# Kernel tuning notes

Hardware: AMD Instinct MI355X
Metric: run time of the kernel (lower is better)

## Reference

```python
import jax, jax.numpy as jnp
import numpy as np

N_NODES = 100000


def _sage_conv(x, edge_index, W_l, W_r, b):
    # PyG SAGEConv (aggr='mean', root_weight=True, bias in lin_l):
    # out_i = W_l @ mean_{j in N(i)} x_j + b + W_r @ x_i
    src = edge_index[0]
    dst = edge_index[1]
    msg = x[src]                                              # [E, d] gather
    agg = jax.ops.segment_sum(msg, dst, num_segments=N_NODES)  # [N, d]
    deg = jax.ops.segment_sum(jnp.ones((src.shape[0],), x.dtype), dst,
                              num_segments=N_NODES)            # [N]
    agg = agg / jnp.maximum(deg, 1.0)[:, None]                 # mean, 0 if isolated
    return agg @ W_l.T + b + x @ W_r.T


def setup_inputs() -> dict:
    key = jax.random.key(0)
    ks = jax.random.split(key, 10)
    E, P = 1600000, 200000
    d_in, d_hid, d_out = 64, 128, 64
    s = 0.05
    return {
        "x": jax.random.normal(ks[0], (N_NODES, d_in), jnp.float32),
        "edge_index": jax.random.randint(ks[1], (2, E), 0, N_NODES, jnp.int32).astype(jnp.int64),
        "pairs": jax.random.randint(ks[2], (P, 2), 0, N_NODES, jnp.int32).astype(jnp.int64),
        "W1l": jax.random.normal(ks[3], (d_hid, d_in), jnp.float32) * s,
        "W1r": jax.random.normal(ks[4], (d_hid, d_in), jnp.float32) * s,
        "b1": jnp.zeros((d_hid,), jnp.float32),
        "W2l": jax.random.normal(ks[5], (d_out, d_hid), jnp.float32) * s,
        "W2r": jax.random.normal(ks[6], (d_out, d_hid), jnp.float32) * s,
        "b2": jnp.zeros((d_out,), jnp.float32),
        "Wlp": jax.random.normal(ks[7], (1, 2 * d_out), jnp.float32) * s,
        "blp": jnp.zeros((1,), jnp.float32),
    }


def reference(x, edge_index, pairs, W1l, W1r, b1, W2l, W2r, b2, Wlp, blp):
    h = _sage_conv(x, edge_index, W1l, W1r, b1)
    h = jax.nn.relu(h)
    h = _sage_conv(h, edge_index, W2l, W2r, b2)          # [N, d_out]
    src_emb = h[pairs[:, 0]]                              # [P, d_out]
    dst_emb = h[pairs[:, 1]]                              # [P, d_out]
    edge_emb = jnp.concatenate([src_emb, dst_emb], axis=1)  # [P, 2*d_out]
    logits = edge_emb @ Wlp.T + blp                       # [P, 1]
    return jax.nn.sigmoid(logits).squeeze(-1)             # [P]
```

## Files before the change

### kernel.cpp

```cpp
#include <hip/hip_runtime.h>


typedef __attribute__((ext_vector_type(8))) short bf16x8;
typedef __attribute__((ext_vector_type(4))) float f32x4;

#define NBLK_A 256

__device__ __forceinline__ unsigned short f2bf(float f) {
    unsigned u = __float_as_uint(f);
    u = u + 0x7fffu + ((u >> 16) & 1u);
    return (unsigned short)(u >> 16);
}
__device__ __forceinline__ float b2f(unsigned short s) {
    return __uint_as_float(((unsigned)s) << 16);
}
__device__ __forceinline__ float uflo(unsigned v) { return __uint_as_float(v << 16); }
__device__ __forceinline__ float ufhi(unsigned v) { return __uint_as_float(v & 0xffff0000u); }

__device__ __forceinline__ long load_idx(const void* p, long i, int is64) {
    if (is64) return (long)((const long long*)p)[i];
    return (long)((const int*)p)[i];
}

__device__ __forceinline__ int detect64_local(const void* p) {
    const unsigned* u = (const unsigned*)p;
    unsigned a = 0;
#pragma unroll
    for (int i = 0; i < 32; ++i) a |= u[2 * i + 1];
    return a == 0u;
}

__global__ void pre_kernel(const void* eidx, const float* __restrict__ x,
                           const float* __restrict__ W1l, const float* __restrict__ W1r,
                           const float* __restrict__ W2l, const float* __restrict__ W2r,
                           const float* __restrict__ b2, const float* __restrict__ Wlp,
                           const float* __restrict__ blp,
                           int* __restrict__ blk_hist, unsigned short* __restrict__ xaown,
                           unsigned short* __restrict__ w1bf, float* __restrict__ wv,
                           int* __restrict__ flag,
                           long N, long E, int NBK, int chunk, int xcb) {
    int b = blockIdx.x;
    int tid = threadIdx.x;
    if (b < NBLK_A) {
        __shared__ int h[512];
        for (int i = tid; i < NBK; i += 256) h[i] = 0;
        __syncthreads();
        int is64 = detect64_local(eidx);
        long e0 = (long)b * chunk;
        long e1 = e0 + chunk; if (e1 > E) e1 = E;
        for (long e = e0 + tid; e < e1; e += 256) {
            long dst = load_idx(eidx, E + e, is64);
            atomicAdd(&h[(int)(dst >> 8)], 1);
        }
        __syncthreads();
        for (int i = tid; i < NBK; i += 256) blk_hist[i * NBLK_A + b] = h[i];
    } else if (b < NBLK_A + xcb) {
        long t = (long)(b - NBLK_A) * 256 + tid;
        long n = t >> 4;
        int q = (int)(t & 15);
        if (n >= N) return;
        float4 v = *(const float4*)&x[n * 64 + q * 4];
        uint2 u;
        u.x = (unsigned)f2bf(v.x) | ((unsigned)f2bf(v.y) << 16);
        u.y = (unsigned)f2bf(v.z) | ((unsigned)f2bf(v.w) << 16);
        *(uint2*)&xaown[n * 64 + q * 4] = u;
    } else {
        if (tid == 0) *flag = detect64_local(eidx);
        if (tid < 128) {
            int k = tid;
            float s0 = 0.f, s1 = 0.f, s2 = 0.f, s3 = 0.f;
            for (int o = 0; o < 64; ++o) {
                float wl = Wlp[o], wr = Wlp[64 + o];
                float l = W2l[o * 128 + k], r = W2r[o * 128 + k];
                s0 += wl * l; s1 += wr * l; s2 += wl * r; s3 += wr * r;
            }
            wv[k] = s0; wv[128 + k] = s1; wv[256 + k] = s2; wv[384 + k] = s3;
            if (k == 0) {
                float c = blp[0];
                for (int o = 0; o < 64; ++o) c += (Wlp[o] + Wlp[64 + o]) * b2[o];
                wv[512] = c;
            }
        }
        for (int i = tid; i < 16384; i += 256) {
            int o = i >> 7, k = i & 127;
            float f = (k < 64) ? W1l[o * 64 + k] : W1r[o * 64 + (k - 64)];
            w1bf[i ^ ((o & 7) << 3)] = f2bf(f);
        }
    }
}

__global__ void bucket_relscan_kernel(int* __restrict__ blk_hist, int* __restrict__ total) {
    __shared__ int ts[256];
    int k = blockIdx.x, t = threadIdx.x;
    int v = blk_hist[k * NBLK_A + t];
    ts[t] = v; __syncthreads();
    for (int off = 1; off < 256; off <<= 1) {
        int u = (t >= off) ? ts[t - off] : 0;
        __syncthreads();
        ts[t] += u;
        __syncthreads();
    }
    blk_hist[k * NBLK_A + t] = ts[t] - v;
    if (t == 255) total[k] = ts[255];
}

__global__ void base_kernel(const int* __restrict__ total, int* __restrict__ base,
                            int* __restrict__ row_start, int NBK, long N, long E) {
    __shared__ int ts[256];
    int t = threadIdx.x;
    int a = (t < NBK) ? total[t] : 0;
    int b = (256 + t < NBK) ? total[256 + t] : 0;
    ts[t] = a; __syncthreads();
    for (int off = 1; off < 256; off <<= 1) {
        int u = (t >= off) ? ts[t - off] : 0;
        __syncthreads();
        ts[t] += u;
        __syncthreads();
    }
    int incl1 = ts[t];
    int sum1 = ts[255];
    if (t < NBK) base[t] = incl1 - a;
    __syncthreads();
    ts[t] = b; __syncthreads();
    for (int off = 1; off < 256; off <<= 1) {
        int u = (t >= off) ? ts[t - off] : 0;
        __syncthreads();
        ts[t] += u;
        __syncthreads();
    }
    int incl2 = ts[t];
    if (256 + t < NBK) base[256 + t] = sum1 + incl2 - b;
    if (t == 255) base[NBK] = sum1 + incl2;
    if (t == 0) row_start[N] = (int)E;
}

__global__ void bucket_scatter_kernel(const void* eidx, const int* flag,
                                      const int* __restrict__ blk_hist, const int* __restrict__ base,
                                      unsigned* __restrict__ ebuf, long E, int NBK, int chunk) {
    __shared__ int cur[512];
    int tid = threadIdx.x, b = blockIdx.x;
    for (int i = tid; i < NBK; i += 256) cur[i] = blk_hist[i * NBLK_A + b] + base[i];
    __syncthreads();
    int is64 = *flag;
    long e0 = (long)b * chunk;
    long e1 = e0 + chunk; if (e1 > E) e1 = E;
    for (long e = e0 + tid; e < e1; e += 256) {
        long src = load_idx(eidx, e, is64);
        long dst = load_idx(eidx, E + e, is64);
        int pos = atomicAdd(&cur[(int)(dst >> 8)], 1);
        ebuf[pos] = (unsigned)src | ((unsigned)(dst & 255) << 24);
    }
}

__global__ void bucket_csr_kernel(const unsigned* __restrict__ ebuf, const int* __restrict__ base,
                                  int* __restrict__ csr_src, int* __restrict__ row_start, long N) {
    __shared__ int cnt[256], sc[256], cur[256];
    int k = blockIdx.x, t = threadIdx.x;
    int bstart = base[k], bend = base[k + 1];
    cnt[t] = 0;
    __syncthreads();
    for (int i = bstart + t; i < bend; i += 256)
        atomicAdd(&cnt[ebuf[i] >> 24], 1);
    __syncthreads();
    int c = cnt[t];
    sc[t] = c; __syncthreads();
    for (int off = 1; off < 256; off <<= 1) {
        int u = (t >= off) ? sc[t - off] : 0;
        __syncthreads();
        sc[t] += u;
        __syncthreads();
    }
    int loff = sc[t] - c;
    cur[t] = loff;
    long n = (long)k * 256 + t;
    if (n < N) row_start[n] = bstart + loff;
    __syncthreads();
    for (int i = bstart + t; i < bend; i += 256) {
        unsigned v = ebuf[i];
        int dl = (int)(v >> 24);
        int p = atomicAdd(&cur[dl], 1);
        csr_src[bstart + p] = (int)(v & 0xFFFFFFu);
    }
}

__global__ __launch_bounds__(512, 4) void fused_gg_kernel(
        const int* __restrict__ rs, const int* __restrict__ csr,
        const unsigned short* __restrict__ xaown,
        const unsigned short* __restrict__ w1bf, const float* __restrict__ b1,
        const float* __restrict__ wv,
        float* __restrict__ ab, float* __restrict__ cd, long N) {
    __shared__ __align__(16) unsigned short wbuf[128 * 128];
    __shared__ __align__(16) unsigned short aggt[8][16 * 64];
    __shared__ float bs1[128];
    __shared__ float wvs[512];
    int tid = threadIdx.x;

    {
        const uint4* src = (const uint4*)w1bf;
        uint4* dst = (uint4*)wbuf;
#pragma unroll
        for (int i = 0; i < 4; ++i) dst[tid + i * 512] = src[tid + i * 512];
    }
    if (tid < 128) bs1[tid] = b1[tid];
    wvs[tid] = wv[tid];

    int lane = tid & 63, wid = tid >> 6;
    int l16 = lane & 15, lg = lane >> 4;
    long n0 = (long)blockIdx.x * 128 + wid * 16;
    unsigned short* agg = aggt[wid];
    unsigned boff = (unsigned)l16 * 4u;

    for (int nl = 0; nl < 16; ++nl) {
        long n = n0 + nl;
        int s = 0, e = 0;
        if (n < N) { s = rs[n]; e = rs[n + 1]; }
        float a0 = 0.f, a1 = 0.f, a2 = 0.f, a3 = 0.f;
        int j = s;
        for (; j + 16 <= e; j += 16) {
            unsigned o0 = ((unsigned)csr[j + lg] << 6) | boff;
            unsigned o1 = ((unsigned)csr[j + 4 + lg] << 6) | boff;
            unsigned o2 = ((unsigned)csr[j + 8 + lg] << 6) | boff;
            unsigned o3 = ((unsigned)csr[j + 12 + lg] << 6) | boff;
            uint2 r0 = *(const uint2*)&xaown[o0];
            uint2 r1 = *(const uint2*)&xaown[o1];
            uint2 r2 = *(const uint2*)&xaown[o2];
            uint2 r3 = *(const uint2*)&xaown[o3];
            a0 += uflo(r0.x); a1 += ufhi(r0.x); a2 += uflo(r0.y); a3 += ufhi(r0.y);
            a0 += uflo(r1.x); a1 += ufhi(r1.x); a2 += uflo(r1.y); a3 += ufhi(r1.y);
            a0 += uflo(r2.x); a1 += ufhi(r2.x); a2 += uflo(r2.y); a3 += ufhi(r2.y);
            a0 += uflo(r3.x); a1 += ufhi(r3.x); a2 += uflo(r3.y); a3 += ufhi(r3.y);
        }
        if (j < e) {
#pragma unroll
            for (int t = 0; t < 4; ++t) {
                int pos = j + 4 * t + lg;
                int ok = pos < e;
                unsigned oo = ((unsigned)csr[ok ? pos : s] << 6) | boff;
                uint2 r = *(const uint2*)&xaown[oo];
                float m = ok ? 1.f : 0.f;
                a0 += m * uflo(r.x); a1 += m * ufhi(r.x);
                a2 += m * uflo(r.y); a3 += m * ufhi(r.y);
            }
        }
        a0 += __shfl_xor(a0, 16, 64);  a1 += __shfl_xor(a1, 16, 64);
        a2 += __shfl_xor(a2, 16, 64);  a3 += __shfl_xor(a3, 16, 64);
        a0 += __shfl_xor(a0, 32, 64);  a1 += __shfl_xor(a1, 32, 64);
        a2 += __shfl_xor(a2, 32, 64);  a3 += __shfl_xor(a3, 32, 64);
        if (lg == 0) {
            float inv = 1.0f / fmaxf((float)(e - s), 1.0f);
            uint2 o;
            o.x = (unsigned)f2bf(a0 * inv) | ((unsigned)f2bf(a1 * inv) << 16);
            o.y = (unsigned)f2bf(a2 * inv) | ((unsigned)f2bf(a3 * inv) << 16);
            int eo = (l16 * 4) ^ ((nl & 7) << 3);
            *(uint2*)&agg[nl * 64 + eo] = o;
        }
    }
    __syncthreads();

    f32x4 acc[8];
#pragma unroll
    for (int ot = 0; ot < 8; ++ot) acc[ot] = (f32x4){0.f, 0.f, 0.f, 0.f};
    const unsigned short* A0 = xaown + (n0 + l16) * 64;
#pragma unroll
    for (int ks = 0; ks < 4; ++ks) {
        int k0 = ks * 32;
        bf16x8 a;
        if (ks < 2) a = *(const bf16x8*)&agg[l16 * 64 + ((k0 + 8 * lg) ^ ((l16 & 7) << 3))];
        else        a = *(const bf16x8*)&A0[(k0 - 64) + 8 * lg];
#pragma unroll
        for (int ot = 0; ot < 8; ++ot) {
            int o = ot * 16 + l16;
            bf16x8 b = *(const bf16x8*)&wbuf[(o * 128 + k0 + 8 * lg) ^ ((o & 7) << 3)];
            acc[ot] = __builtin_amdgcn_mfma_f32_16x16x32_bf16(a, b, acc[ot], 0, 0, 0);
        }
    }

#pragma unroll
    for (int j = 0; j < 4; ++j) {
        float da = 0.f, db = 0.f, dc = 0.f, dd = 0.f;
#pragma unroll
        for (int ot = 0; ot < 8; ++ot) {
            int col = ot * 16 + l16;
            float hv = fmaxf(acc[ot][j] + bs1[col], 0.f);
            da += hv * wvs[col];       db += hv * wvs[128 + col];
            dc += hv * wvs[256 + col]; dd += hv * wvs[384 + col];
        }
        da += __shfl_xor(da, 1, 64); db += __shfl_xor(db, 1, 64);
        dc += __shfl_xor(dc, 1, 64); dd += __shfl_xor(dd, 1, 64);
        da += __shfl_xor(da, 2, 64); db += __shfl_xor(db, 2, 64);
        dc += __shfl_xor(dc, 2, 64); dd += __shfl_xor(dd, 2, 64);
        da += __shfl_xor(da, 4, 64); db += __shfl_xor(db, 4, 64);
        dc += __shfl_xor(dc, 4, 64); dd += __shfl_xor(dd, 4, 64);
        da += __shfl_xor(da, 8, 64); db += __shfl_xor(db, 8, 64);
        dc += __shfl_xor(dc, 8, 64); dd += __shfl_xor(dd, 8, 64);
        long n = n0 + lg * 4 + j;
        if (l16 == 0 && n < N) {
            *(float2*)&ab[n * 2] = make_float2(da, db);
            *(float2*)&cd[n * 2] = make_float2(dc, dd);
        }
    }
}

__global__ void sgather_kernel(const int* __restrict__ rs, const int* __restrict__ csr,
                               const float* __restrict__ ab, const float* __restrict__ cd,
                               float* __restrict__ UV, long N) {
    long n = (long)blockIdx.x * 256 + threadIdx.x;
    if (n >= N) return;
    int s = rs[n], e = rs[n + 1];
    float sa = 0.f, sb = 0.f;
    int j = s;
    for (; j + 4 <= e; j += 4) {
        unsigned i0 = (unsigned)csr[j] * 2u, i1 = (unsigned)csr[j + 1] * 2u;
        unsigned i2 = (unsigned)csr[j + 2] * 2u, i3 = (unsigned)csr[j + 3] * 2u;
        float2 v0 = *(const float2*)&ab[i0];
        float2 v1 = *(const float2*)&ab[i1];
        float2 v2 = *(const float2*)&ab[i2];
        float2 v3 = *(const float2*)&ab[i3];
        sa += (v0.x + v1.x) + (v2.x + v3.x);
        sb += (v0.y + v1.y) + (v2.y + v3.y);
    }
    for (; j < e; ++j) {
        float2 v = *(const float2*)&ab[(unsigned)csr[j] * 2u];
        sa += v.x; sb += v.y;
    }
    float inv = 1.0f / fmaxf((float)(e - s), 1.0f);
    float2 cdv = *(const float2*)&cd[n * 2];
    *(float2*)&UV[n * 2] = make_float2(sa * inv + cdv.x, sb * inv + cdv.y);
}

__global__ void linkpred_kernel(const void* pairs, const int* flag,
                                const float* __restrict__ UV, const float* __restrict__ wv,
                                float* __restrict__ out, long P) {
    long p = (long)blockIdx.x * 256 + threadIdx.x;
    if (p >= P) return;
    int is64 = *flag;
    long s = load_idx(pairs, 2 * p, is64);
    long d = load_idx(pairs, 2 * p + 1, is64);
    float acc = UV[s * 2] + UV[d * 2 + 1] + wv[512];
    out[p] = 1.0f / (1.0f + expf(-acc));
}

extern "C" void kernel_launch(void* const* d_in, const int* in_sizes, int n_in,
                              void* d_out, int out_size, void* d_ws, size_t ws_size,
                              hipStream_t stream) {
    const float* x    = (const float*)d_in[0];
    const void*  eidx  = d_in[1];
    const void*  pairs = d_in[2];
    const float* W1l = (const float*)d_in[3];
    const float* W1r = (const float*)d_in[4];
    const float* b1  = (const float*)d_in[5];
    const float* W2l = (const float*)d_in[6];
    const float* W2r = (const float*)d_in[7];
    const float* b2  = (const float*)d_in[8];
    const float* Wlp = (const float*)d_in[9];
    const float* blp = (const float*)d_in[10];
    float* out = (float*)d_out;

    long N = in_sizes[0] / 64;
    long E = in_sizes[1] / 2;
    long P = in_sizes[2] / 2;
    long NP = (N + 127) & ~127L;
    int NBK = (int)((N + 255) >> 8);
    int chunk = (int)((E + NBLK_A - 1) / NBLK_A);
    int xcb = (int)((N * 16 + 255) / 256);

    char* w = (char*)d_ws;
    auto alloc = [&](size_t bytes) {
        char* p = w;
        w += (bytes + 255) & ~(size_t)255;
        return p;
    };
    int* row_start = (int*)alloc((N + 1) * sizeof(int));
    int* csr_src   = (int*)alloc(E * sizeof(int));
    int* blk_hist  = (int*)alloc((size_t)NBK * NBLK_A * sizeof(int));
    int* total     = (int*)alloc(NBK * sizeof(int));
    int* base      = (int*)alloc((NBK + 1) * sizeof(int));
    int* flag      = (int*)alloc(64);
    unsigned* ebuf = (unsigned*)alloc(E * sizeof(unsigned));
    unsigned short* xaown = (unsigned short*)alloc((size_t)NP * 64 * 2);
    unsigned short* w1bf  = (unsigned short*)alloc(16384 * 2);
    float* ab = (float*)alloc((size_t)N * 2 * sizeof(float));
    float* cd = (float*)alloc((size_t)N * 2 * sizeof(float));
    float* UV = (float*)alloc((size_t)N * 2 * sizeof(float));
    float* wv = (float*)alloc(1024 * sizeof(float));

    unsigned pre_blocks = (unsigned)(NBLK_A + xcb + 1);
    pre_kernel<<<pre_blocks, 256, 0, stream>>>(eidx, x, W1l, W1r, W2l, W2r, b2, Wlp, blp,
                                               blk_hist, xaown, w1bf, wv, flag,
                                               N, E, NBK, chunk, xcb);

    bucket_relscan_kernel<<<NBK, 256, 0, stream>>>(blk_hist, total);
    base_kernel<<<1, 256, 0, stream>>>(total, base, row_start, NBK, N, E);
    bucket_scatter_kernel<<<NBLK_A, 256, 0, stream>>>(eidx, flag, blk_hist, base, ebuf, E, NBK, chunk);
    bucket_csr_kernel<<<NBK, 256, 0, stream>>>(ebuf, base, csr_src, row_start, N);

    unsigned gblocks = (unsigned)(NP / 128);
    fused_gg_kernel<<<gblocks, 512, 0, stream>>>(row_start, csr_src, xaown, w1bf, b1, wv, ab, cd, N);

    unsigned sgblocks = (unsigned)((N + 255) / 256);
    sgather_kernel<<<sgblocks, 256, 0, stream>>>(row_start, csr_src, ab, cd, UV, N);

    unsigned pblocks = (unsigned)((P + 255) / 256);
    linkpred_kernel<<<pblocks, 256, 0, stream>>>(pairs, flag, UV, wv, out, P);
}
```

Measured before the change: 148.3 us.

## Split fused neighbor-gather and GEMM into separate per-node gather and GEMM kernels

The neighbor mean-aggregation moves out of the fused gather+GEMM kernel into its own kernel. There, one wavefront handles each node instead of each wave walking 16 nodes in sequence. The bf16 aggregated features go to a new global buffer, which the GEMM kernel then reads directly instead of from swizzled LDS. The aim is to expose far more memory-level parallelism for the latency-bound irregular gather. The cost is an extra kernel launch, a round trip of the aggregated features through global memory, and an occupancy hint dropped from the GEMM's launch bounds.

```diff
diff --git a/kernel.cpp b/kernel.cpp
--- a/kernel.cpp
+++ b/kernel.cpp
@@ -183,14 +183,64 @@
     }
 }
 
-__global__ __launch_bounds__(512, 4) void fused_gg_kernel(
-        const int* __restrict__ rs, const int* __restrict__ csr,
-        const unsigned short* __restrict__ xaown,
+__global__ void gather_kernel(const int* __restrict__ rs, const int* __restrict__ csr,
+                              const unsigned short* __restrict__ T,
+                              unsigned short* __restrict__ Out, long N) {
+    long gid = (long)blockIdx.x * 256 + threadIdx.x;
+    long n = gid >> 6;
+    if (n >= N) return;
+    int lane = (int)(gid & 63);
+    int lg = lane >> 4;
+    int fq = lane & 15;
+    int s = rs[n], e = rs[n + 1];
+    unsigned boff = (unsigned)fq * 4u;
+    float a0 = 0.f, a1 = 0.f, a2 = 0.f, a3 = 0.f;
+    int j = s;
+    for (; j + 16 <= e; j += 16) {
+        unsigned o0 = ((unsigned)csr[j + lg] << 6) | boff;
+        unsigned o1 = ((unsigned)csr[j + 4 + lg] << 6) | boff;
+        unsigned o2 = ((unsigned)csr[j + 8 + lg] << 6) | boff;
+        unsigned o3 = ((unsigned)csr[j + 12 + lg] << 6) | boff;
+        uint2 r0 = *(const uint2*)&T[o0];
+        uint2 r1 = *(const uint2*)&T[o1];
+        uint2 r2 = *(const uint2*)&T[o2];
+        uint2 r3 = *(const uint2*)&T[o3];
+        a0 += uflo(r0.x); a1 += ufhi(r0.x); a2 += uflo(r0.y); a3 += ufhi(r0.y);
+        a0 += uflo(r1.x); a1 += ufhi(r1.x); a2 += uflo(r1.y); a3 += ufhi(r1.y);
+        a0 += uflo(r2.x); a1 += ufhi(r2.x); a2 += uflo(r2.y); a3 += ufhi(r2.y);
+        a0 += uflo(r3.x); a1 += ufhi(r3.x); a2 += uflo(r3.y); a3 += ufhi(r3.y);
+    }
+    if (j < e) {
+#pragma unroll
+        for (int t = 0; t < 4; ++t) {
+            int pos = j + 4 * t + lg;
+            int ok = pos < e;
+            unsigned oo = ((unsigned)csr[ok ? pos : s] << 6) | boff;
+            uint2 r = *(const uint2*)&T[oo];
+            float m = ok ? 1.f : 0.f;
+            a0 += m * uflo(r.x); a1 += m * ufhi(r.x);
+            a2 += m * uflo(r.y); a3 += m * ufhi(r.y);
+        }
+    }
+    a0 += __shfl_xor(a0, 16, 64);  a1 += __shfl_xor(a1, 16, 64);
+    a2 += __shfl_xor(a2, 16, 64);  a3 += __shfl_xor(a3, 16, 64);
+    a0 += __shfl_xor(a0, 32, 64);  a1 += __shfl_xor(a1, 32, 64);
+    a2 += __shfl_xor(a2, 32, 64);  a3 += __shfl_xor(a3, 32, 64);
+    if (lg == 0) {
+        float inv = 1.0f / fmaxf((float)(e - s), 1.0f);
+        uint2 o;
+        o.x = (unsigned)f2bf(a0 * inv) | ((unsigned)f2bf(a1 * inv) << 16);
+        o.y = (unsigned)f2bf(a2 * inv) | ((unsigned)f2bf(a3 * inv) << 16);
+        *(uint2*)&Out[((unsigned)n << 6) | boff] = o;
+    }
+}
+
+__global__ __launch_bounds__(512) void fused_gemm_kernel(
+        const unsigned short* __restrict__ xagg, const unsigned short* __restrict__ xaown,
         const unsigned short* __restrict__ w1bf, const float* __restrict__ b1,
         const float* __restrict__ wv,
         float* __restrict__ ab, float* __restrict__ cd, long N) {
     __shared__ __align__(16) unsigned short wbuf[128 * 128];
-    __shared__ __align__(16) unsigned short aggt[8][16 * 64];
     __shared__ float bs1[128];
     __shared__ float wvs[512];
     int tid = threadIdx.x;
@@ -203,70 +253,24 @@
     }
     if (tid < 128) bs1[tid] = b1[tid];
     wvs[tid] = wv[tid];
+    __syncthreads();
 
     int lane = tid & 63, wid = tid >> 6;
     int l16 = lane & 15, lg = lane >> 4;
     long n0 = (long)blockIdx.x * 128 + wid * 16;
-    unsigned short* agg = aggt[wid];
-    unsigned boff = (unsigned)l16 * 4u;
-
-    for (int nl = 0; nl < 16; ++nl) {
-        long n = n0 + nl;
-        int s = 0, e = 0;
-        if (n < N) { s = rs[n]; e = rs[n + 1]; }
-        float a0 = 0.f, a1 = 0.f, a2 = 0.f, a3 = 0.f;
-        int j = s;
-        for (; j + 16 <= e; j += 16) {
-            unsigned o0 = ((unsigned)csr[j + lg] << 6) | boff;
-            unsigned o1 = ((unsigned)csr[j + 4 + lg] << 6) | boff;
-            unsigned o2 = ((unsigned)csr[j + 8 + lg] << 6) | boff;
-            unsigned o3 = ((unsigned)csr[j + 12 + lg] << 6) | boff;
-            uint2 r0 = *(const uint2*)&xaown[o0];
-            uint2 r1 = *(const uint2*)&xaown[o1];
-            uint2 r2 = *(const uint2*)&xaown[o2];
-            uint2 r3 = *(const uint2*)&xaown[o3];
-            a0 += uflo(r0.x); a1 += ufhi(r0.x); a2 += uflo(r0.y); a3 += ufhi(r0.y);
-            a0 += uflo(r1.x); a1 += ufhi(r1.x); a2 += uflo(r1.y); a3 += ufhi(r1.y);
-            a0 += uflo(r2.x); a1 += ufhi(r2.x); a2 += uflo(r2.y); a3 += ufhi(r2.y);
-            a0 += uflo(r3.x); a1 += ufhi(r3.x); a2 += uflo(r3.y); a3 += ufhi(r3.y);
-        }
-        if (j < e) {
-#pragma unroll
-            for (int t = 0; t < 4; ++t) {
-                int pos = j + 4 * t + lg;
-                int ok = pos < e;
-                unsigned oo = ((unsigned)csr[ok ? pos : s] << 6) | boff;
-                uint2 r = *(const uint2*)&xaown[oo];
-                float m = ok ? 1.f : 0.f;
-                a0 += m * uflo(r.x); a1 += m * ufhi(r.x);
-                a2 += m * uflo(r.y); a3 += m * ufhi(r.y);
-            }
-        }
-        a0 += __shfl_xor(a0, 16, 64);  a1 += __shfl_xor(a1, 16, 64);
-        a2 += __shfl_xor(a2, 16, 64);  a3 += __shfl_xor(a3, 16, 64);
-        a0 += __shfl_xor(a0, 32, 64);  a1 += __shfl_xor(a1, 32, 64);
-        a2 += __shfl_xor(a2, 32, 64);  a3 += __shfl_xor(a3, 32, 64);
-        if (lg == 0) {
-            float inv = 1.0f / fmaxf((float)(e - s), 1.0f);
-            uint2 o;
-            o.x = (unsigned)f2bf(a0 * inv) | ((unsigned)f2bf(a1 * inv) << 16);
-            o.y = (unsigned)f2bf(a2 * inv) | ((unsigned)f2bf(a3 * inv) << 16);
-            int eo = (l16 * 4) ^ ((nl & 7) << 3);
-            *(uint2*)&agg[nl * 64 + eo] = o;
-        }
-    }
-    __syncthreads();
+    const unsigned short* Ag = xagg + (n0 + l16) * 64;
+    const unsigned short* Ao = xaown + (n0 + l16) * 64;
 
     f32x4 acc[8];
 #pragma unroll
     for (int ot = 0; ot < 8; ++ot) acc[ot] = (f32x4){0.f, 0.f, 0.f, 0.f};
-    const unsigned short* A0 = xaown + (n0 + l16) * 64;
+
 #pragma unroll
     for (int ks = 0; ks < 4; ++ks) {
         int k0 = ks * 32;
         bf16x8 a;
-        if (ks < 2) a = *(const bf16x8*)&agg[l16 * 64 + ((k0 + 8 * lg) ^ ((l16 & 7) << 3))];
-        else        a = *(const bf16x8*)&A0[(k0 - 64) + 8 * lg];
+        if (ks < 2) a = *(const bf16x8*)&Ag[k0 + 8 * lg];
+        else        a = *(const bf16x8*)&Ao[(k0 - 64) + 8 * lg];
 #pragma unroll
         for (int ot = 0; ot < 8; ++ot) {
             int o = ot * 16 + l16;
@@ -378,6 +382,7 @@
     int* flag      = (int*)alloc(64);
     unsigned* ebuf = (unsigned*)alloc(E * sizeof(unsigned));
     unsigned short* xaown = (unsigned short*)alloc((size_t)NP * 64 * 2);
+    unsigned short* xagg  = (unsigned short*)alloc((size_t)NP * 64 * 2);
     unsigned short* w1bf  = (unsigned short*)alloc(16384 * 2);
     float* ab = (float*)alloc((size_t)N * 2 * sizeof(float));
     float* cd = (float*)alloc((size_t)N * 2 * sizeof(float));
@@ -394,8 +399,11 @@
     bucket_scatter_kernel<<<NBLK_A, 256, 0, stream>>>(eidx, flag, blk_hist, base, ebuf, E, NBK, chunk);
     bucket_csr_kernel<<<NBK, 256, 0, stream>>>(ebuf, base, csr_src, row_start, N);
 
+    unsigned gth_blocks = (unsigned)((N * 64 + 255) / 256);
+    gather_kernel<<<gth_blocks, 256, 0, stream>>>(row_start, csr_src, xaown, xagg, N);
+
     unsigned gblocks = (unsigned)(NP / 128);
-    fused_gg_kernel<<<gblocks, 512, 0, stream>>>(row_start, csr_src, xaown, w1bf, b1, wv, ab, cd, N);
+    fused_gemm_kernel<<<gblocks, 512, 0, stream>>>(xagg, xaown, w1bf, b1, wv, ab, cd, N);
 
     unsigned sgblocks = (unsigned)((N + 255) / 256);
     sgather_kernel<<<sgblocks, 256, 0, stream>>>(row_start, csr_src, ab, cd, UV, N);
```

Result: faster. 131.7 us, median of 2 (-11.2%).
